# Performance work log

Hardware: AMD Instinct MI355X
Metric: run time of the kernel (lower is better)

Reference implementation:

```python
import jax, jax.numpy as jnp
import numpy as np

NUM_HEADS = 32
HEAD_DIM = 128  # 4096 / 32


def setup_inputs() -> dict:
    key = jax.random.key(0)
    k1, k2, k3 = jax.random.split(key, 3)
    B, S, H = 1, 2048, 4096
    hidden_states = jax.random.normal(k1, (B, S, H), dtype=jnp.float32)
    # causal additive mask, broadcast over heads: 0 on/below diagonal, large negative above
    neg = jnp.finfo(jnp.float32).min
    causal = jnp.triu(jnp.full((S, S), neg, dtype=jnp.float32), k=1)
    attention_mask = causal[None, None, :, :]  # [1,1,S,S]
    w_pack = jax.random.normal(k2, (3 * H, H), dtype=jnp.float32) * 0.02
    w_o = jax.random.normal(k3, (H, H), dtype=jnp.float32) * 0.02
    return {"hidden_states": hidden_states, "attention_mask": attention_mask,
            "w_pack": w_pack, "w_o": w_o}


def reference(hidden_states, attention_mask, w_pack, w_o):
    B, S, H = hidden_states.shape
    nh, hd = NUM_HEADS, HEAD_DIM
    # fused QKV projection (Linear, no bias): x @ W^T
    proj = hidden_states @ w_pack.T                      # [B,S,3H]
    q, k, v = jnp.split(proj, 3, axis=-1)
    q = q.reshape(B, S, nh, hd).transpose(0, 2, 1, 3)    # [B,nh,S,hd]
    k = k.reshape(B, S, nh, hd).transpose(0, 2, 1, 3)
    v = v.reshape(B, S, nh, hd).transpose(0, 2, 1, 3)
    scale = 1.0 / jnp.sqrt(jnp.float32(hd))
    attn = jnp.einsum('bhqd,bhkd->bhqk', q, k) * scale   # [B,nh,S,S]
    attn = attn + attention_mask
    attn = jnp.maximum(attn, jnp.finfo(attn.dtype).min)  # clamp like torch.max(..., finfo.min)
    attn = jax.nn.softmax(attn, axis=-1)
    out = jnp.einsum('bhqk,bhkd->bhqd', attn, v)         # [B,nh,S,hd]
    out = out.transpose(0, 2, 1, 3).reshape(B, S, nh * hd)
    return out @ w_o.T                                    # [B,S,H]
```

## Files before the change

kernel.cpp:

```cpp
#include <hip/hip_runtime.h>
#include <stdint.h>

typedef __attribute__((ext_vector_type(8))) short short8;
typedef __attribute__((ext_vector_type(4))) float floatx4;

#define SEQ    2048
#define HID    4096
#define NHEAD  32
#define HDIMV  128
#define PROJN  12288

__device__ __forceinline__ unsigned short f2bf(float f) {
  union { float f; unsigned u; } v; v.f = f;
  unsigned r = (v.u + 0x7fffu + ((v.u >> 16) & 1u)) >> 16;
  return (unsigned short)r;
}

__device__ __forceinline__ void g2l16(const void* g, void* l) {
  __builtin_amdgcn_global_load_lds(
      (const __attribute__((address_space(1))) void*)g,
      (__attribute__((address_space(3))) void*)l, 16, 0, 0);
}

__global__ __launch_bounds__(256) void pack_fp32(const float* __restrict__ src,
                                                 unsigned short* __restrict__ dst, int K) {
  const int rp = blockIdx.x, kt = blockIdx.y, t = threadIdx.x;
  const long tb = ((long)rp * gridDim.y + kt) * 8192;
#pragma unroll
  for (int j = 0; j < 4; j++) {
    int ch = t + j * 256;
    int r = ch & 127, cc = ch >> 7;
    const float* s = src + (long)(rp * 128 + r) * K + kt * 64 + cc * 8;
    float4 a = *(const float4*)s;
    float4 b = *(const float4*)(s + 4);
    short8 o;
    o[0] = (short)f2bf(a.x); o[1] = (short)f2bf(a.y);
    o[2] = (short)f2bf(a.z); o[3] = (short)f2bf(a.w);
    o[4] = (short)f2bf(b.x); o[5] = (short)f2bf(b.y);
    o[6] = (short)f2bf(b.z); o[7] = (short)f2bf(b.w);
    *(short8*)(dst + tb + ch * 8) = o;
  }
}

__global__ __launch_bounds__(256) void pack_qk(const unsigned short* __restrict__ proj,
                                               unsigned short* __restrict__ dstQ,
                                               unsigned short* __restrict__ dstK) {
  const int st = blockIdx.x, h = blockIdx.y, t = threadIdx.x;
  const long tb = ((long)(h * 16 + st)) * 16384;
#pragma unroll
  for (int j = 0; j < 8; j++) {
    int ch = t + j * 256;
    int r = ch & 127, cc = ch >> 7;
    long so = (long)(st * 128 + r) * PROJN + h * 128 + cc * 8;
    *(short8*)(dstQ + tb + ch * 8) = *(const short8*)(proj + so);
    *(short8*)(dstK + tb + ch * 8) = *(const short8*)(proj + so + HID);
  }
}

__global__ __launch_bounds__(256) void pack_v(const unsigned short* __restrict__ proj,
                                              unsigned short* __restrict__ Vf) {
  __shared__ unsigned short T[128 * 136];
  const int st = blockIdx.x, h = blockIdx.y, t = threadIdx.x;
  const long tb = ((long)(h * 16 + st)) * 16384;
  const unsigned short* src = proj + (long)(st * 128) * PROJN + 2 * HID + h * 128;
#pragma unroll
  for (int it = 0; it < 8; it++) {
    int idx = t * 8 + it * 2048;
    int r = idx >> 7, c = idx & 127;
    *(short8*)(T + r * 136 + c) = *(const short8*)(src + (long)r * PROJN + c);
  }
  __syncthreads();
#pragma unroll
  for (int pass = 0; pass < 4; pass++) {
    int d = (t >> 3) + pass * 32;
    int sc = t & 7;
    short8 lo, hi;
#pragma unroll
    for (int j = 0; j < 8; j++) lo[j] = (short)T[(sc * 16 + j) * 136 + d];
#pragma unroll
    for (int j = 0; j < 8; j++) hi[j] = (short)T[(sc * 16 + 8 + j) * 136 + d];
    *(short8*)(Vf + tb + ((sc * 2) * 128 + d) * 8) = lo;
    *(short8*)(Vf + tb + ((sc * 2 + 1) * 128 + d) * 8) = hi;
  }
}

template<int OUT_F32>
__global__ __launch_bounds__(256, 4) void gemm_pk(
    const unsigned short* __restrict__ Ap,
    const unsigned short* __restrict__ Bp,
    void* __restrict__ C, int N, int K) {
  __shared__ __align__(16) unsigned short As[8192];
  __shared__ __align__(16) unsigned short Bs[8192];
  const int t = threadIdx.x;
  const int wave = t >> 6, lane = t & 63;
  const int bid = blockIdx.x;
  const int xcd = bid & 7;
  const int li = bid >> 3;
  const int mi = li & 15;
  const int ni = (li >> 4) * 8 + xcd;
  const int KT = K >> 6;
  const unsigned short* at = Ap + (long)mi * KT * 8192 + t * 8;
  const unsigned short* bt = Bp + (long)ni * KT * 8192 + t * 8;
  unsigned short* asl = As + wave * 512;
  unsigned short* bsl = Bs + wave * 512;

  const int mw = (wave >> 1) * 64;
  const int nw = (wave & 1) * 64;
  const int lq = lane & 15, lg = lane >> 4;

  floatx4 zero = {0.f, 0.f, 0.f, 0.f};
  floatx4 acc[4][4];
  for (int i = 0; i < 4; i++)
    for (int j = 0; j < 4; j++) acc[i][j] = zero;

  for (int kt = 0; kt < KT; kt++) {
    __syncthreads();
    const unsigned short* ak = at + (long)kt * 8192;
    const unsigned short* bk = bt + (long)kt * 8192;
#pragma unroll
    for (int j = 0; j < 4; j++) g2l16(ak + j * 2048, asl + j * 2048);
#pragma unroll
    for (int j = 0; j < 4; j++) g2l16(bk + j * 2048, bsl + j * 2048);
    __syncthreads();
#pragma unroll
    for (int kk = 0; kk < 2; kk++) {
      const int ch = (kk * 4 + lg) * 1024;
      short8 af[4], bfr[4];
#pragma unroll
      for (int i = 0; i < 4; i++)
        af[i] = *(const short8*)(As + ch + (mw + i * 16 + lq) * 8);
#pragma unroll
      for (int j = 0; j < 4; j++)
        bfr[j] = *(const short8*)(Bs + ch + (nw + j * 16 + lq) * 8);
#pragma unroll
      for (int i = 0; i < 4; i++)
#pragma unroll
        for (int j = 0; j < 4; j++)
          acc[i][j] = __builtin_amdgcn_mfma_f32_16x16x32_bf16(af[i], bfr[j], acc[i][j], 0, 0, 0);
    }
  }

  const int row0 = mi * 128 + mw + lg * 4;
  const int col0 = ni * 128 + nw + lq;
  if (OUT_F32) {
    float* Cf = (float*)C;
#pragma unroll
    for (int i = 0; i < 4; i++)
#pragma unroll
      for (int j = 0; j < 4; j++)
#pragma unroll
        for (int r = 0; r < 4; r++)
          Cf[(long)(row0 + i * 16 + r) * N + col0 + j * 16] = acc[i][j][r];
  } else {
    unsigned short* Cb = (unsigned short*)C;
#pragma unroll
    for (int i = 0; i < 4; i++)
#pragma unroll
      for (int j = 0; j < 4; j++)
#pragma unroll
        for (int r = 0; r < 4; r++)
          Cb[(long)(row0 + i * 16 + r) * N + col0 + j * 16] = f2bf(acc[i][j][r]);
  }
}

__global__ __launch_bounds__(256, 2) void attn_kernel(
    const unsigned short* __restrict__ Qf,
    const unsigned short* __restrict__ Kf,
    const unsigned short* __restrict__ Vf,
    unsigned short* __restrict__ aop) {
  __shared__ __align__(16) unsigned short Ps[16384];
  const int bx = blockIdx.x;
  const int h = bx & 31;
  const int qt = 15 - (bx >> 5);
  const int t = threadIdx.x, wave = t >> 6, lane = t & 63;
  const int lq = lane & 15, lg = lane >> 4;
  const int wOff = wave * 32;
  const float scale2 = 0.12751744154f;

  const unsigned short* qb = Qf + ((long)(h * 16 + qt)) * 16384;
  short8 qf[2][4];
#pragma unroll
  for (int i = 0; i < 2; i++)
#pragma unroll
    for (int kk = 0; kk < 4; kk++)
      qf[i][kk] = *(const short8*)(qb + ((kk * 4 + lg) * 128 + wOff + i * 16 + lq) * 8);

  float mraw[2][4], lsum[2][4];
  floatx4 zero = {0.f, 0.f, 0.f, 0.f};
  floatx4 o[2][8];
#pragma unroll
  for (int i = 0; i < 2; i++)
#pragma unroll
    for (int r = 0; r < 4; r++) { mraw[i][r] = -INFINITY; lsum[i][r] = 0.f; }
#pragma unroll
  for (int i = 0; i < 2; i++)
#pragma unroll
    for (int j = 0; j < 8; j++) o[i][j] = zero;

  for (int kv = 0; kv <= qt; kv++) {
    const bool diag = (kv == qt);
    const unsigned short* kb = Kf + ((long)(h * 16 + kv)) * 16384;
    const unsigned short* vb = Vf + ((long)(h * 16 + kv)) * 16384;

    floatx4 s[2][8];
#pragma unroll
    for (int i = 0; i < 2; i++)
#pragma unroll
      for (int j = 0; j < 8; j++) s[i][j] = zero;
#pragma unroll
    for (int kk = 0; kk < 4; kk++) {
      short8 bfr[8];
#pragma unroll
      for (int j = 0; j < 8; j++)
        bfr[j] = *(const short8*)(kb + ((kk * 4 + lg) * 128 + j * 16 + lq) * 8);
#pragma unroll
      for (int i = 0; i < 2; i++)
#pragma unroll
        for (int j = 0; j < 8; j++)
          s[i][j] = __builtin_amdgcn_mfma_f32_16x16x32_bf16(qf[i][kk], bfr[j], s[i][j], 0, 0, 0);
    }

    if (diag) {
#pragma unroll
      for (int i = 0; i < 2; i++)
#pragma unroll
        for (int r = 0; r < 4; r++) {
          int qrow = qt * 128 + wOff + i * 16 + lg * 4 + r;
#pragma unroll
          for (int j = 0; j < 8; j++)
            if (kv * 128 + j * 16 + lq > qrow) s[i][j][r] = -INFINITY;
        }
    }

    float alpha_[2][4];
#pragma unroll
    for (int i = 0; i < 2; i++) {
#pragma unroll
      for (int r = 0; r < 4; r++) {
        float mx = s[i][0][r];
#pragma unroll
        for (int j = 1; j < 8; j++) mx = fmaxf(mx, s[i][j][r]);
#pragma unroll
        for (int d = 1; d < 16; d <<= 1) mx = fmaxf(mx, __shfl_xor(mx, d, 64));
        float mnew = fmaxf(mraw[i][r], mx);
        float al = exp2f((mraw[i][r] - mnew) * scale2);
        float c = mnew * scale2;
        float ps = 0.f;
#pragma unroll
        for (int j = 0; j < 8; j++) {
          float p = exp2f(fmaf(s[i][j][r], scale2, -c));
          s[i][j][r] = p;
          ps += p;
        }
#pragma unroll
        for (int d = 1; d < 16; d <<= 1) ps += __shfl_xor(ps, d, 64);
        lsum[i][r] = lsum[i][r] * al + ps;
        mraw[i][r] = mnew;
        alpha_[i][r] = al;
      }
    }
#pragma unroll
    for (int i = 0; i < 2; i++)
#pragma unroll
      for (int j = 0; j < 8; j++)
#pragma unroll
        for (int r = 0; r < 4; r++) o[i][j][r] *= alpha_[i][r];

#pragma unroll
    for (int i = 0; i < 2; i++)
#pragma unroll
      for (int r = 0; r < 4; r++) {
        int prow = wOff + i * 16 + lg * 4 + r;
#pragma unroll
        for (int j = 0; j < 8; j++)
          Ps[((j * 2 + (lq >> 3)) * 128 + prow) * 8 + (lq & 7)] = f2bf(s[i][j][r]);
      }

#pragma unroll
    for (int kk = 0; kk < 4; kk++) {
      short8 pf[2], vf[8];
#pragma unroll
      for (int i = 0; i < 2; i++)
        pf[i] = *(const short8*)(Ps + ((kk * 4 + lg) * 128 + wOff + i * 16 + lq) * 8);
#pragma unroll
      for (int j = 0; j < 8; j++)
        vf[j] = *(const short8*)(vb + ((kk * 4 + lg) * 128 + j * 16 + lq) * 8);
#pragma unroll
      for (int i = 0; i < 2; i++)
#pragma unroll
        for (int j = 0; j < 8; j++)
          o[i][j] = __builtin_amdgcn_mfma_f32_16x16x32_bf16(pf[i], vf[j], o[i][j], 0, 0, 0);
    }
  }

#pragma unroll
  for (int i = 0; i < 2; i++) {
    float inv[4];
#pragma unroll
    for (int r = 0; r < 4; r++) inv[r] = 1.0f / lsum[i][r];
#pragma unroll
    for (int r = 0; r < 4; r++) {
      int prow = wOff + i * 16 + lg * 4 + r;
#pragma unroll
      for (int j = 0; j < 8; j++)
        Ps[((j * 2 + (lq >> 3)) * 128 + prow) * 8 + (lq & 7)] = f2bf(o[i][j][r] * inv[r]);
    }
  }
#pragma unroll
  for (int it = 0; it < 8; it++) {
    int row_loc = it * 4 + (lane >> 4);
    int cc = lane & 15;
    short8 v = *(const short8*)(Ps + (cc * 128 + wOff + row_loc) * 8);
    long tb = ((long)qt * 64 + h * 2 + (cc >> 3)) * 8192;
    *(short8*)(aop + tb + ((cc & 7) * 128 + wOff + row_loc) * 8) = v;
  }
}

extern "C" void kernel_launch(void* const* d_in, const int* in_sizes, int n_in,
                              void* d_out, int out_size, void* d_ws, size_t ws_size,
                              hipStream_t stream) {
  (void)in_sizes; (void)n_in; (void)out_size;
  const float* hs = (const float*)d_in[0];
  const float* wp = (const float*)d_in[2];
  const float* wo = (const float*)d_in[3];
  float* out = (float*)d_out;
  char* ws = (char*)d_ws;

  unsigned short* Ap1  = (unsigned short*)(ws);
  unsigned short* Bp1  = (unsigned short*)(ws + 16777216);
  unsigned short* Bp2  = (unsigned short*)(ws + 117440512);
  unsigned short* proj = (unsigned short*)(ws + 150994944);
  unsigned short* aop  = (unsigned short*)(ws + 201326592);
  unsigned short* Qf   = (unsigned short*)(ws);
  unsigned short* Kf   = (unsigned short*)(ws + 16777216);
  unsigned short* Vf   = (unsigned short*)(ws + 33554432);
  if (ws_size < 218103808) return;

  pack_fp32<<<dim3(16, 64), 256, 0, stream>>>(hs, Ap1, HID);
  pack_fp32<<<dim3(96, 64), 256, 0, stream>>>(wp, Bp1, HID);
  pack_fp32<<<dim3(32, 64), 256, 0, stream>>>(wo, Bp2, HID);

  gemm_pk<0><<<1536, 256, 0, stream>>>(Ap1, Bp1, (void*)proj, PROJN, HID);

  pack_qk<<<dim3(16, 32), 256, 0, stream>>>(proj, Qf, Kf);
  pack_v<<<dim3(16, 32), 256, 0, stream>>>(proj, Vf);

  attn_kernel<<<512, 256, 0, stream>>>(Qf, Kf, Vf, aop);

  gemm_pk<1><<<512, 256, 0, stream>>>(aop, Bp2, (void*)out, HID, HID);
}
```

Before: 966.1 us.

## Double-buffer K/V tiles in LDS and fold softmax scale into Q weights

The attention kernel now stages each K and V tile into shared memory with async global-to-LDS loads, double-buffered so the next tile loads while the current one is computed. Previously every wave read K/V fragments straight from global memory. The softmax scale (1/sqrt(d)·log2e) is folded into the Q rows of the packed QKV weight, which removes per-element multiplies in the exp2 path. The extra 128KB of LDS forces launch bounds down to one block per CU, and a barrier is added each iteration.

```diff
diff --git a/kernel.cpp b/kernel.cpp
--- a/kernel.cpp
+++ b/kernel.cpp
@@ -23,21 +23,23 @@
 }
 
 __global__ __launch_bounds__(256) void pack_fp32(const float* __restrict__ src,
-                                                 unsigned short* __restrict__ dst, int K) {
+                                                 unsigned short* __restrict__ dst, int K,
+                                                 int scale_rows, float scale) {
   const int rp = blockIdx.x, kt = blockIdx.y, t = threadIdx.x;
   const long tb = ((long)rp * gridDim.y + kt) * 8192;
 #pragma unroll
   for (int j = 0; j < 4; j++) {
     int ch = t + j * 256;
     int r = ch & 127, cc = ch >> 7;
+    float sc = (rp * 128 + r < scale_rows) ? scale : 1.0f;
     const float* s = src + (long)(rp * 128 + r) * K + kt * 64 + cc * 8;
     float4 a = *(const float4*)s;
     float4 b = *(const float4*)(s + 4);
     short8 o;
-    o[0] = (short)f2bf(a.x); o[1] = (short)f2bf(a.y);
-    o[2] = (short)f2bf(a.z); o[3] = (short)f2bf(a.w);
-    o[4] = (short)f2bf(b.x); o[5] = (short)f2bf(b.y);
-    o[6] = (short)f2bf(b.z); o[7] = (short)f2bf(b.w);
+    o[0] = (short)f2bf(a.x * sc); o[1] = (short)f2bf(a.y * sc);
+    o[2] = (short)f2bf(a.z * sc); o[3] = (short)f2bf(a.w * sc);
+    o[4] = (short)f2bf(b.x * sc); o[5] = (short)f2bf(b.y * sc);
+    o[6] = (short)f2bf(b.z * sc); o[7] = (short)f2bf(b.w * sc);
     *(short8*)(dst + tb + ch * 8) = o;
   }
 }
@@ -163,11 +165,21 @@
   }
 }
 
-__global__ __launch_bounds__(256, 2) void attn_kernel(
+__device__ __forceinline__ void stage_tile(const unsigned short* g, unsigned short* lds,
+                                           int wave, int lane) {
+  const unsigned short* gp = g + wave * 4096 + lane * 8;
+  unsigned short* lp = lds + wave * 4096;
+#pragma unroll
+  for (int j = 0; j < 8; j++) g2l16(gp + j * 512, lp + j * 512);
+}
+
+__global__ __launch_bounds__(256, 1) void attn_kernel(
     const unsigned short* __restrict__ Qf,
     const unsigned short* __restrict__ Kf,
     const unsigned short* __restrict__ Vf,
     unsigned short* __restrict__ aop) {
+  __shared__ __align__(16) unsigned short Ks[2][16384];
+  __shared__ __align__(16) unsigned short Vs[2][16384];
   __shared__ __align__(16) unsigned short Ps[16384];
   const int bx = blockIdx.x;
   const int h = bx & 31;
@@ -175,7 +187,6 @@
   const int t = threadIdx.x, wave = t >> 6, lane = t & 63;
   const int lq = lane & 15, lg = lane >> 4;
   const int wOff = wave * 32;
-  const float scale2 = 0.12751744154f;
 
   const unsigned short* qb = Qf + ((long)(h * 16 + qt)) * 16384;
   short8 qf[2][4];
@@ -197,10 +208,19 @@
 #pragma unroll
     for (int j = 0; j < 8; j++) o[i][j] = zero;
 
+  const unsigned short* kb0 = Kf + ((long)h * 16) * 16384;
+  const unsigned short* vb0 = Vf + ((long)h * 16) * 16384;
+  stage_tile(kb0, Ks[0], wave, lane);
+  stage_tile(vb0, Vs[0], wave, lane);
+
   for (int kv = 0; kv <= qt; kv++) {
+    const int cur = kv & 1;
     const bool diag = (kv == qt);
-    const unsigned short* kb = Kf + ((long)(h * 16 + kv)) * 16384;
-    const unsigned short* vb = Vf + ((long)(h * 16 + kv)) * 16384;
+    __syncthreads();
+    if (!diag) {
+      stage_tile(kb0 + (long)(kv + 1) * 16384, Ks[1 - cur], wave, lane);
+      stage_tile(vb0 + (long)(kv + 1) * 16384, Vs[1 - cur], wave, lane);
+    }
 
     floatx4 s[2][8];
 #pragma unroll
@@ -212,7 +232,7 @@
       short8 bfr[8];
 #pragma unroll
       for (int j = 0; j < 8; j++)
-        bfr[j] = *(const short8*)(kb + ((kk * 4 + lg) * 128 + j * 16 + lq) * 8);
+        bfr[j] = *(const short8*)(&Ks[cur][((kk * 4 + lg) * 128 + j * 16 + lq) * 8]);
 #pragma unroll
       for (int i = 0; i < 2; i++)
 #pragma unroll
@@ -243,12 +263,11 @@
 #pragma unroll
         for (int d = 1; d < 16; d <<= 1) mx = fmaxf(mx, __shfl_xor(mx, d, 64));
         float mnew = fmaxf(mraw[i][r], mx);
-        float al = exp2f((mraw[i][r] - mnew) * scale2);
-        float c = mnew * scale2;
+        float al = exp2f(mraw[i][r] - mnew);
         float ps = 0.f;
 #pragma unroll
         for (int j = 0; j < 8; j++) {
-          float p = exp2f(fmaf(s[i][j][r], scale2, -c));
+          float p = exp2f(s[i][j][r] - mnew);
           s[i][j][r] = p;
           ps += p;
         }
@@ -284,7 +303,7 @@
         pf[i] = *(const short8*)(Ps + ((kk * 4 + lg) * 128 + wOff + i * 16 + lq) * 8);
 #pragma unroll
       for (int j = 0; j < 8; j++)
-        vf[j] = *(const short8*)(vb + ((kk * 4 + lg) * 128 + j * 16 + lq) * 8);
+        vf[j] = *(const short8*)(&Vs[cur][((kk * 4 + lg) * 128 + j * 16 + lq) * 8]);
 #pragma unroll
       for (int i = 0; i < 2; i++)
 #pragma unroll
@@ -336,9 +355,9 @@
   unsigned short* Vf   = (unsigned short*)(ws + 33554432);
   if (ws_size < 218103808) return;
 
-  pack_fp32<<<dim3(16, 64), 256, 0, stream>>>(hs, Ap1, HID);
-  pack_fp32<<<dim3(96, 64), 256, 0, stream>>>(wp, Bp1, HID);
-  pack_fp32<<<dim3(32, 64), 256, 0, stream>>>(wo, Bp2, HID);
+  pack_fp32<<<dim3(16, 64), 256, 0, stream>>>(hs, Ap1, HID, 0, 1.0f);
+  pack_fp32<<<dim3(96, 64), 256, 0, stream>>>(wp, Bp1, HID, 4096, 0.12751744154f);
+  pack_fp32<<<dim3(32, 64), 256, 0, stream>>>(wo, Bp2, HID, 0, 1.0f);
 
   gemm_pk<0><<<1536, 256, 0, stream>>>(Ap1, Bp1, (void*)proj, PROJN, HID);
 
```

Result: faster. 785.7 us (-18.7%).
